# Kernel tuning notes

Hardware: AMD Instinct MI355X
Metric: run time of the kernel (lower is better)

## Reference

```python
import jax, jax.numpy as jnp
import numpy as np


def dequant_weight(cb, idx):
    """Reconstruct weight from product-quantization codebooks.
    cb:  [C, K, sub]  codebooks
    idx: [C, out]     int codes per codebook per output row
    returns W: [out, C*sub]
    """
    C = cb.shape[0]
    gathered = cb[jnp.arange(C)[:, None], idx]          # [C, out, sub]
    W = jnp.transpose(gathered, (1, 0, 2))               # [out, C, sub]
    return W.reshape(W.shape[0], -1)                     # [out, C*sub]


def setup_inputs() -> dict:
    key = jax.random.key(0)
    ks = jax.random.split(key, 7)
    B, S, D, H, C, K = 4, 2048, 1024, 4096, 8, 256
    return {
        "x": jax.random.normal(ks[0], (B, S, D), dtype=jnp.float32),
        "cb1": jax.random.normal(ks[1], (C, K, D // C), dtype=jnp.float32) * 0.02,
        "idx1": jax.random.randint(ks[2], (C, H), 0, K, dtype=jnp.int32),
        "b1": jax.random.normal(ks[3], (H,), dtype=jnp.float32) * 0.02,
        "cb2": jax.random.normal(ks[4], (C, K, H // C), dtype=jnp.float32) * 0.02,
        "idx2": jax.random.randint(ks[5], (C, D), 0, K, dtype=jnp.int32),
        "b2": jax.random.normal(ks[6], (D,), dtype=jnp.float32) * 0.02,
    }


def reference(x, cb1, idx1, b1, cb2, idx2, b2):
    # fc1: dequantize W1 [hidden, dim] from shared codebooks, then linear
    W1 = dequant_weight(cb1, idx1)                       # [H, D]
    h = jnp.einsum("bsd,hd->bsh", x, W1) + b1            # [B, S, H]
    h = jax.nn.gelu(h, approximate=False)                # exact GELU (torch default)
    # fc2: dequantize W2 [dim, hidden], linear back to dim
    W2 = dequant_weight(cb2, idx2)                       # [D, H]
    return jnp.einsum("bsh,dh->bsd", h, W2) + b2         # [B, S, D]
```

## Files before the change

kernel.cpp:

```cpp
#include <hip/hip_runtime.h>
#include <hip/hip_bf16.h>
#include <math.h>

typedef __bf16 bf16_t;
typedef bf16_t bf16x8 __attribute__((ext_vector_type(8)));
typedef float f32x4 __attribute__((ext_vector_type(4)));
typedef unsigned short u16x8 __attribute__((ext_vector_type(8)));

__device__ __forceinline__ void g2l16(const bf16_t* g, bf16_t* l) {
    __builtin_amdgcn_global_load_lds(
        (const __attribute__((address_space(1))) void*)g,
        (__attribute__((address_space(3))) void*)l, 16, 0, 0);
}

__global__ void prep_all(const void* __restrict__ x,
                         const void* __restrict__ cb1, const int* __restrict__ idx1,
                         const void* __restrict__ b1,
                         const void* __restrict__ cb2, const int* __restrict__ idx2,
                         const void* __restrict__ b2,
                         bf16_t* __restrict__ xb, bf16_t* __restrict__ w1b,
                         bf16_t* __restrict__ w2b, float* __restrict__ b1f,
                         float* __restrict__ b2f, int* __restrict__ flag, int M) {
    __shared__ int s_bad;
    const int t = threadIdx.x;
    if (t == 0) s_bad = 0;
    __syncthreads();
    {
        u16x8 v = ((const u16x8*)x)[t];
        int cnt = 0;
#pragma unroll
        for (int j = 0; j < 8; ++j) cnt += (((v[j] >> 7) & 0xFF) >= 0x88);
#pragma unroll
        for (int o = 32; o > 0; o >>= 1) cnt += __shfl_down(cnt, o, 64);
        if ((t & 63) == 0) atomicAdd(&s_bad, cnt);
    }
    __syncthreads();
    const int f32 = (s_bad > 4);
    if (blockIdx.x == 0 && t == 0) flag[0] = f32;

    const int bX = M >> 3;
    const int b = blockIdx.x;

    if (b < bX) {
        const int c0 = b * 1024 + t;
        if (f32) {
            const float4* p = (const float4*)x;
#pragma unroll
            for (int k = 0; k < 4; ++k) {
                const int ci = c0 + k * 256;
                float4 a = p[2 * ci], bb = p[2 * ci + 1];
                bf16x8 o;
                o[0] = (bf16_t)a.x;  o[1] = (bf16_t)a.y;
                o[2] = (bf16_t)a.z;  o[3] = (bf16_t)a.w;
                o[4] = (bf16_t)bb.x; o[5] = (bf16_t)bb.y;
                o[6] = (bf16_t)bb.z; o[7] = (bf16_t)bb.w;
                *(bf16x8*)(xb + (size_t)ci * 8) = o;
            }
        } else {
            const bf16x8* p = (const bf16x8*)x;
#pragma unroll
            for (int k = 0; k < 4; ++k) {
                const int ci = c0 + k * 256;
                *(bf16x8*)(xb + (size_t)ci * 8) = p[ci];
            }
        }
        return;
    }

    int wb = b - bX;
    if (wb < 512) {
        const int c0 = wb * 1024 + t;
        if (f32) {
#pragma unroll
            for (int k = 0; k < 4; ++k) {
                const int ii = c0 + k * 256;
                const int r = ii >> 7;
                const int col = (ii & 127) << 3;
                const int cc = col >> 7;
                const int code = idx1[cc * 4096 + r];
                const float* s = (const float*)cb1 + (size_t)(cc * 256 + code) * 128 + (col & 127);
                float4 a = *(const float4*)s, bb = *(const float4*)(s + 4);
                bf16x8 o;
                o[0] = (bf16_t)a.x;  o[1] = (bf16_t)a.y;
                o[2] = (bf16_t)a.z;  o[3] = (bf16_t)a.w;
                o[4] = (bf16_t)bb.x; o[5] = (bf16_t)bb.y;
                o[6] = (bf16_t)bb.z; o[7] = (bf16_t)bb.w;
                *(bf16x8*)(w1b + (size_t)r * 1024 + col) = o;
            }
        } else {
#pragma unroll
            for (int k = 0; k < 4; ++k) {
                const int ii = c0 + k * 256;
                const int r = ii >> 7;
                const int col = (ii & 127) << 3;
                const int cc = col >> 7;
                const int code = idx1[cc * 4096 + r];
                *(bf16x8*)(w1b + (size_t)r * 1024 + col) =
                    *(const bf16x8*)((const bf16_t*)cb1 + (size_t)(cc * 256 + code) * 128 + (col & 127));
            }
        }
        return;
    }

    wb -= 512;
    {
        const int c0 = wb * 1024 + t;
        if (f32) {
#pragma unroll
            for (int k = 0; k < 4; ++k) {
                const int ii = c0 + k * 256;
                const int r = ii >> 9;
                const int col = (ii & 511) << 3;
                const int cc = col >> 9;
                const int code = idx2[cc * 1024 + r];
                const float* s = (const float*)cb2 + (size_t)(cc * 256 + code) * 512 + (col & 511);
                float4 a = *(const float4*)s, bb = *(const float4*)(s + 4);
                bf16x8 o;
                o[0] = (bf16_t)a.x;  o[1] = (bf16_t)a.y;
                o[2] = (bf16_t)a.z;  o[3] = (bf16_t)a.w;
                o[4] = (bf16_t)bb.x; o[5] = (bf16_t)bb.y;
                o[6] = (bf16_t)bb.z; o[7] = (bf16_t)bb.w;
                *(bf16x8*)(w2b + (size_t)r * 4096 + col) = o;
            }
        } else {
#pragma unroll
            for (int k = 0; k < 4; ++k) {
                const int ii = c0 + k * 256;
                const int r = ii >> 9;
                const int col = (ii & 511) << 3;
                const int cc = col >> 9;
                const int code = idx2[cc * 1024 + r];
                *(bf16x8*)(w2b + (size_t)r * 4096 + col) =
                    *(const bf16x8*)((const bf16_t*)cb2 + (size_t)(cc * 256 + code) * 512 + (col & 511));
            }
        }
    }

    if (wb == 511) {
        for (int g = t; g < 640; g += 256) {
#pragma unroll
            for (int j = 0; j < 8; ++j) {
                const int e = g * 8 + j;
                const void* src = (e < 4096) ? b1 : b2;
                const int k = (e < 4096) ? e : e - 4096;
                const float v = f32 ? ((const float*)src)[k]
                                    : (float)(((const bf16_t*)src)[k]);
                if (e < 4096) b1f[k] = v; else b2f[k] = v;
            }
        }
    }
}

template <bool XCDSW, bool GELU, bool DYNOUT>
__global__ __launch_bounds__(256, 2)
void gemm_bt(const bf16_t* __restrict__ A, const bf16_t* __restrict__ Bw,
             const float* __restrict__ bias,
             bf16_t* __restrict__ obf, float* __restrict__ of32,
             int M, int N, int K, const int* __restrict__ flag) {
    __shared__ __attribute__((aligned(16))) bf16_t sA[128 * 64];
    __shared__ __attribute__((aligned(16))) bf16_t sB[128 * 64];

    const int tid = threadIdx.x;

    int bm, bn;
    if (XCDSW) {
        const int l = blockIdx.y * gridDim.x + blockIdx.x;
        const int xcd = l & 7;
        const int i = l >> 3;
        const int per = gridDim.y >> 3;
        bm = (xcd * per + (i % per)) << 7;
        bn = (i / per) << 7;
    } else {
        bm = blockIdx.y << 7;
        bn = blockIdx.x << 7;
    }

    const int row0 = tid >> 3;
    const int kc0 = ((tid & 7) - row0) & 7;
    const bf16_t* gA = A + (size_t)(bm + row0) * K + kc0 * 8;
    const bf16_t* gB = Bw + (size_t)(bn + row0) * K + kc0 * 8;
    bf16_t* lA = sA + tid * 8;
    bf16_t* lB = sB + tid * 8;
    const size_t pskip = (size_t)32 * K;

    const int lane = tid & 63;
    const int wave = tid >> 6;
    const int quad = lane >> 4;
    const int lr = lane & 15;
    const int wm = (wave & 1) << 6;
    const int wn = (wave >> 1) << 6;

    const int arow = wm + lr;
    const int brow = wn + lr;
    const bf16x8* pA0 = (const bf16x8*)(sA + arow * 64 + ((quad + arow) & 7) * 8);
    const bf16x8* pA1 = (const bf16x8*)(sA + arow * 64 + ((quad + 4 + arow) & 7) * 8);
    const bf16x8* pB0 = (const bf16x8*)(sB + brow * 64 + ((quad + brow) & 7) * 8);
    const bf16x8* pB1 = (const bf16x8*)(sB + brow * 64 + ((quad + 4 + brow) & 7) * 8);

    f32x4 acc[4][4] = {};

    for (int k0 = 0; k0 < K; k0 += 64) {
#pragma unroll
        for (int p = 0; p < 4; ++p) g2l16(gA + p * pskip + k0, lA + p * 2048);
#pragma unroll
        for (int p = 0; p < 4; ++p) g2l16(gB + p * pskip + k0, lB + p * 2048);
        __syncthreads();

        bf16x8 af[4], bf[4];
#pragma unroll
        for (int f = 0; f < 4; ++f) { af[f] = pA0[f * 128]; bf[f] = pB0[f * 128]; }
#pragma unroll
        for (int mi = 0; mi < 4; ++mi)
#pragma unroll
            for (int ni = 0; ni < 4; ++ni)
                acc[mi][ni] = __builtin_amdgcn_mfma_f32_16x16x32_bf16(
                    af[mi], bf[ni], acc[mi][ni], 0, 0, 0);
#pragma unroll
        for (int f = 0; f < 4; ++f) { af[f] = pA1[f * 128]; bf[f] = pB1[f * 128]; }
#pragma unroll
        for (int mi = 0; mi < 4; ++mi)
#pragma unroll
            for (int ni = 0; ni < 4; ++ni)
                acc[mi][ni] = __builtin_amdgcn_mfma_f32_16x16x32_bf16(
                    af[mi], bf[ni], acc[mi][ni], 0, 0, 0);
        __syncthreads();
    }

    const int outf32 = DYNOUT ? *flag : 0;
#pragma unroll
    for (int mi = 0; mi < 4; ++mi) {
#pragma unroll
        for (int ni = 0; ni < 4; ++ni) {
            const int n = bn + wn + ni * 16 + lr;
            const float bs = bias[n];
            f32x4 v = acc[mi][ni];
#pragma unroll
            for (int r = 0; r < 4; ++r) {
                const int m = bm + wm + mi * 16 + quad * 4 + r;
                float val = v[r] + bs;
                if (GELU) val = 0.5f * val * (1.0f + erff(val * 0.70710678118654752f));
                const size_t o = (size_t)m * N + n;
                if (DYNOUT) {
                    if (outf32) of32[o] = val;
                    else        obf[o] = (bf16_t)val;
                } else {
                    obf[o] = (bf16_t)val;
                }
            }
        }
    }
}

extern "C" void kernel_launch(void* const* d_in, const int* in_sizes, int n_in,
                              void* d_out, int out_size, void* d_ws, size_t ws_size,
                              hipStream_t stream) {
    const void* x   = d_in[0];
    const void* cb1 = d_in[1];
    const int*  idx1 = (const int*)d_in[2];
    const void* b1  = d_in[3];
    const void* cb2 = d_in[4];
    const int*  idx2 = (const int*)d_in[5];
    const void* b2  = d_in[6];

    const int D = 1024, H = 4096;
    const int M = in_sizes[0] / D;

    char* ws = (char*)d_ws;
    bf16_t* xb  = (bf16_t*)ws;
    bf16_t* w1b = (bf16_t*)(ws + (size_t)M * D * 2);
    bf16_t* hb  = (bf16_t*)((char*)w1b + (size_t)H * D * 2);
    bf16_t* w2b = (bf16_t*)((char*)hb + (size_t)M * H * 2);
    float*  b1f = (float*)((char*)w2b + (size_t)D * H * 2);
    float*  b2f = b1f + H;
    int*    flag = (int*)(b2f + D);

    prep_all<<<(M >> 3) + 1024, 256, 0, stream>>>(x, cb1, idx1, b1, cb2, idx2, b2,
                                                  xb, w1b, w2b, b1f, b2f, flag, M);

    dim3 g1(H / 128, M / 128);
    gemm_bt<false, true, false><<<g1, 256, 0, stream>>>(xb, w1b, b1f, hb, nullptr, M, H, D, flag);

    dim3 g2(D / 128, M / 128);
    gemm_bt<true, false, true><<<g2, 256, 0, stream>>>(hb, w2b, b2f,
        (bf16_t*)d_out, (float*)d_out, M, D, H, flag);
}
```

Baseline: 262.7 us.

## Use 256x256 tile, 8-wave pipelined GEMM for fc1

Adds a new GEMM kernel with 256x256 output tiles, 512 threads and double-buffered LDS fed by direct global-to-LDS loads. The kernel staggers its prefetch stages between four MFMA phases and raises wave priority during the MFMA work. It also remaps blocks so each XCD works on a contiguous band of M. The goal is more data reuse per tile and better overlap of loads with compute for the large fc1 GEMM, at the cost of higher register and LDS pressure and fewer blocks per launch. fc2 still uses the old kernel.

Result: no change. 264.0 us (+0.5%).

```diff
diff --git a/kernel.cpp b/kernel.cpp
--- a/kernel.cpp
+++ b/kernel.cpp
@@ -251,6 +251,183 @@
     }
 }
 
+template <bool GELU, bool DYNOUT>
+__global__ __launch_bounds__(512, 2)
+void gemm256(const bf16_t* __restrict__ A, const bf16_t* __restrict__ Bw,
+             const float* __restrict__ bias,
+             bf16_t* __restrict__ obf, float* __restrict__ of32,
+             int M, int N, int K, const int* __restrict__ flag) {
+    __shared__ __attribute__((aligned(16))) bf16_t sA[2 * 256 * 64];
+    __shared__ __attribute__((aligned(16))) bf16_t sB[2 * 256 * 64];
+
+    const int tid = threadIdx.x;
+    const int NT = K >> 6;
+
+    const int l = blockIdx.x;
+    const int nbm = M >> 8;
+    const int per = nbm >> 3;
+    const int xcd = l & 7;
+    const int i = l >> 3;
+    const int bm = (xcd * per + (i % per)) << 8;
+    const int bn = (i / per) << 8;
+
+    const int row0 = tid >> 3;
+    const int kc = ((tid & 7) - row0) & 7;
+    const bf16_t* gA0 = A + (size_t)(bm + row0) * K + kc * 8;
+    const bf16_t* gB0 = Bw + (size_t)(bn + row0) * K + kc * 8;
+    bf16_t* lA0 = sA + tid * 8;
+    bf16_t* lB0 = sB + tid * 8;
+
+#define STAGE_A(off_, h_, kt_) do {                                   \
+    const bf16_t* g_ = gA0 + (size_t)((h_) * 128) * K + (kt_) * 64;   \
+    bf16_t* l_ = lA0 + (off_) + (h_) * 8192;                          \
+    g2l16(g_, l_);                                                    \
+    g2l16(g_ + (size_t)64 * K, l_ + 4096);                            \
+} while (0)
+#define STAGE_B(off_, h_, kt_) do {                                   \
+    const bf16_t* g_ = gB0 + (size_t)((h_) * 128) * K + (kt_) * 64;   \
+    bf16_t* l_ = lB0 + (off_) + (h_) * 8192;                          \
+    g2l16(g_, l_);                                                    \
+    g2l16(g_ + (size_t)64 * K, l_ + 4096);                            \
+} while (0)
+
+    const int lane = tid & 63;
+    const int wave = tid >> 6;
+    const int wm = wave >> 2;
+    const int wn = wave & 3;
+    const int lr = lane & 15;
+    const int quad = lane >> 4;
+    const int c0 = ((quad + lr) & 7) * 8;
+    const int c1 = ((quad + lr + 4) & 7) * 8;
+    const bf16_t* pA = sA + (wm * 128 + lr) * 64;
+    const bf16_t* pB = sB + (wn * 64 + lr) * 64;
+
+    f32x4 acc[8][4] = {};
+    bf16x8 afl[4][2], afh[4][2], bfr[2][2];
+
+    STAGE_A(0, 0, 0); STAGE_A(0, 1, 0); STAGE_B(0, 0, 0); STAGE_B(0, 1, 0);
+    if (NT > 1) { STAGE_A(16384, 0, 1); STAGE_A(16384, 1, 1); STAGE_B(16384, 0, 1); }
+    asm volatile("s_waitcnt vmcnt(6)" ::: "memory");
+    __builtin_amdgcn_s_barrier();
+
+    for (int t = 0; t < NT; ++t) {
+        const int bo = (t & 1) << 14;
+        const int obo = bo ^ 16384;
+
+#pragma unroll
+        for (int mi = 0; mi < 4; ++mi) {
+            afl[mi][0] = *(const bf16x8*)(pA + bo + mi * 1024 + c0);
+            afl[mi][1] = *(const bf16x8*)(pA + bo + mi * 1024 + c1);
+        }
+#pragma unroll
+        for (int j = 0; j < 2; ++j) {
+            bfr[j][0] = *(const bf16x8*)(pB + bo + j * 1024 + c0);
+            bfr[j][1] = *(const bf16x8*)(pB + bo + j * 1024 + c1);
+        }
+        if (t + 1 < NT) STAGE_B(obo, 1, t + 1);
+        __builtin_amdgcn_s_barrier();
+        asm volatile("s_waitcnt lgkmcnt(0)" ::: "memory");
+        __builtin_amdgcn_s_setprio(1);
+#pragma unroll
+        for (int mi = 0; mi < 4; ++mi)
+#pragma unroll
+            for (int j = 0; j < 2; ++j) {
+                acc[mi][j] = __builtin_amdgcn_mfma_f32_16x16x32_bf16(
+                    afl[mi][0], bfr[j][0], acc[mi][j], 0, 0, 0);
+                acc[mi][j] = __builtin_amdgcn_mfma_f32_16x16x32_bf16(
+                    afl[mi][1], bfr[j][1], acc[mi][j], 0, 0, 0);
+            }
+        __builtin_amdgcn_s_setprio(0);
+        __builtin_amdgcn_s_barrier();
+
+#pragma unroll
+        for (int mi = 0; mi < 4; ++mi) {
+            afh[mi][0] = *(const bf16x8*)(pA + bo + (4 + mi) * 1024 + c0);
+            afh[mi][1] = *(const bf16x8*)(pA + bo + (4 + mi) * 1024 + c1);
+        }
+        __builtin_amdgcn_s_barrier();
+        asm volatile("s_waitcnt lgkmcnt(0)" ::: "memory");
+        __builtin_amdgcn_s_setprio(1);
+#pragma unroll
+        for (int mi = 0; mi < 4; ++mi)
+#pragma unroll
+            for (int j = 0; j < 2; ++j) {
+                acc[4 + mi][j] = __builtin_amdgcn_mfma_f32_16x16x32_bf16(
+                    afh[mi][0], bfr[j][0], acc[4 + mi][j], 0, 0, 0);
+                acc[4 + mi][j] = __builtin_amdgcn_mfma_f32_16x16x32_bf16(
+                    afh[mi][1], bfr[j][1], acc[4 + mi][j], 0, 0, 0);
+            }
+        __builtin_amdgcn_s_setprio(0);
+        __builtin_amdgcn_s_barrier();
+
+#pragma unroll
+        for (int j = 0; j < 2; ++j) {
+            bfr[j][0] = *(const bf16x8*)(pB + bo + (2 + j) * 1024 + c0);
+            bfr[j][1] = *(const bf16x8*)(pB + bo + (2 + j) * 1024 + c1);
+        }
+        if (t + 2 < NT) STAGE_A(bo, 0, t + 2);
+        __builtin_amdgcn_s_barrier();
+        asm volatile("s_waitcnt lgkmcnt(0)" ::: "memory");
+        __builtin_amdgcn_s_setprio(1);
+#pragma unroll
+        for (int mi = 0; mi < 4; ++mi)
+#pragma unroll
+            for (int j = 0; j < 2; ++j) {
+                acc[4 + mi][2 + j] = __builtin_amdgcn_mfma_f32_16x16x32_bf16(
+                    afh[mi][0], bfr[j][0], acc[4 + mi][2 + j], 0, 0, 0);
+                acc[4 + mi][2 + j] = __builtin_amdgcn_mfma_f32_16x16x32_bf16(
+                    afh[mi][1], bfr[j][1], acc[4 + mi][2 + j], 0, 0, 0);
+            }
+        __builtin_amdgcn_s_setprio(0);
+        __builtin_amdgcn_s_barrier();
+
+        if (t + 2 < NT) { STAGE_A(bo, 1, t + 2); STAGE_B(bo, 0, t + 2); }
+        __builtin_amdgcn_s_setprio(1);
+#pragma unroll
+        for (int mi = 0; mi < 4; ++mi)
+#pragma unroll
+            for (int j = 0; j < 2; ++j) {
+                acc[mi][2 + j] = __builtin_amdgcn_mfma_f32_16x16x32_bf16(
+                    afl[mi][0], bfr[j][0], acc[mi][2 + j], 0, 0, 0);
+                acc[mi][2 + j] = __builtin_amdgcn_mfma_f32_16x16x32_bf16(
+                    afl[mi][1], bfr[j][1], acc[mi][2 + j], 0, 0, 0);
+            }
+        __builtin_amdgcn_s_setprio(0);
+        if (t + 2 < NT)      asm volatile("s_waitcnt vmcnt(6)" ::: "memory");
+        else if (t + 1 < NT) asm volatile("s_waitcnt vmcnt(0)" ::: "memory");
+        __builtin_amdgcn_s_barrier();
+    }
+
+#undef STAGE_A
+#undef STAGE_B
+
+    const int outf32 = DYNOUT ? *flag : 0;
+    const int mrow = bm + wm * 128 + quad * 4;
+    const int ncol = bn + wn * 64 + lr;
+#pragma unroll
+    for (int mi = 0; mi < 8; ++mi) {
+#pragma unroll
+        for (int j = 0; j < 4; ++j) {
+            const int n = ncol + j * 16;
+            const float bs = bias[n];
+            f32x4 v = acc[mi][j];
+#pragma unroll
+            for (int r = 0; r < 4; ++r) {
+                const int m = mrow + mi * 16 + r;
+                float val = v[r] + bs;
+                if (GELU) val = 0.5f * val * (1.0f + erff(val * 0.70710678118654752f));
+                const size_t o = (size_t)m * N + n;
+                if (DYNOUT) {
+                    if (outf32) of32[o] = val;
+                    else        obf[o] = (bf16_t)val;
+                } else {
+                    obf[o] = (bf16_t)val;
+                }
+            }
+        }
+    }
+}
+
 extern "C" void kernel_launch(void* const* d_in, const int* in_sizes, int n_in,
                               void* d_out, int out_size, void* d_ws, size_t ws_size,
                               hipStream_t stream) {
@@ -277,8 +454,8 @@
     prep_all<<<(M >> 3) + 1024, 256, 0, stream>>>(x, cb1, idx1, b1, cb2, idx2, b2,
                                                   xb, w1b, w2b, b1f, b2f, flag, M);
 
-    dim3 g1(H / 128, M / 128);
-    gemm_bt<false, true, false><<<g1, 256, 0, stream>>>(xb, w1b, b1f, hb, nullptr, M, H, D, flag);
+    gemm256<true, false><<<(M / 256) * (H / 256), 512, 0, stream>>>(
+        xb, w1b, b1f, hb, nullptr, M, H, D, flag);
 
     dim3 g2(D / 128, M / 128);
     gemm_bt<true, false, true><<<g2, 256, 0, stream>>>(hb, w2b, b2f,
```
